# Optimization experiments

Hardware: AMD Instinct MI355X
Metric: run time of the kernel (lower is better)

## Reference

```python
import jax, jax.numpy as jnp
import numpy as np

L_IMG, L_TXT, B, C, T, D = 12, 12, 64, 1000, 8, 512


def setup_inputs() -> dict:
    key = jax.random.key(0)
    ks = jax.random.split(key, 8)
    s = 0.05  # keep attention logits in a sane range
    return {
        "x": jax.random.normal(ks[0], (L_IMG, B, D), jnp.float32),                 # per-layer projected CLS feats [L,B,D]
        "text_features": jax.random.normal(ks[1], (C, L_TXT, T, D), jnp.float32),  # precomputed per-class text feats
        "self_in_w": jax.random.normal(ks[2], (3 * D, D), jnp.float32) * s,
        "self_in_b": jnp.zeros((3 * D,), jnp.float32),
        "self_out_w": jax.random.normal(ks[3], (D, D), jnp.float32) * s,
        "self_out_b": jnp.zeros((D,), jnp.float32),
        "cross_in_w": jax.random.normal(ks[4], (3 * D, D), jnp.float32) * s,
        "cross_in_b": jnp.zeros((3 * D,), jnp.float32),
        "cross_out_w": jax.random.normal(ks[5], (D, D), jnp.float32) * s,
        "cross_out_b": jnp.zeros((D,), jnp.float32),
        "logit_scale": jnp.full((1,), np.log(1.0 / 0.07), jnp.float32),
    }


def reference(x, text_features, self_in_w, self_in_b, self_out_w, self_out_b,
              cross_in_w, cross_in_b, cross_out_w, cross_out_b, logit_scale):
    d = x.shape[-1]
    scale = 1.0 / jnp.sqrt(jnp.asarray(d, x.dtype))

    # ---- self-attention over the layer axis (torch MHA, 1 head, seq-first [L,B,D]) ----
    Wq, Wk, Wv = jnp.split(self_in_w, 3, axis=0)
    bq, bk, bv = jnp.split(self_in_b, 3, axis=0)
    q = jnp.einsum('lbd,ed->lbe', x, Wq) + bq
    k = jnp.einsum('lbd,ed->lbe', x, Wk) + bk
    v = jnp.einsum('lbd,ed->lbe', x, Wv) + bv
    attn = jax.nn.softmax(jnp.einsum('lbe,mbe->blm', q, k) * scale, axis=-1)
    xs = jnp.einsum('blm,mbe->lbe', attn, v) @ self_out_w.T + self_out_b   # [L,B,D]
    image_features = xs[-1]                                               # [B,D]

    # ---- batched cross-attention: query = image layer-tokens, key/value = per-class,
    #      per-template text layer-tokens; averaged over templates and query layers ----
    cWq, cWk, cWv = jnp.split(cross_in_w, 3, axis=0)
    cbq, cbk, cbv = jnp.split(cross_in_b, 3, axis=0)
    q2 = jnp.einsum('lbd,ed->lbe', xs, cWq) + cbq                          # [L,B,E]
    k2 = jnp.einsum('cmtd,ed->cmte', text_features, cWk) + cbk             # [C,M,T,E]
    v2 = jnp.einsum('cmtd,ed->cmte', text_features, cWv) + cbv
    a2 = jax.nn.softmax(jnp.einsum('lbe,cmte->bctlm', q2, k2) * scale, axis=-1)
    n_avg = a2.shape[2] * a2.shape[3]                                      # T * L_img
    # out_proj is linear, so mean over (template, layer) commutes with it
    ctx = jnp.einsum('bctlm,cmtd->bcd', a2, v2) / n_avg                    # [B,C,D]
    txt = ctx @ cross_out_w.T + cross_out_b                                # [B,C,D]

    # ---- normalize and compute logits (matching the source's permute(1,2,0) + norm(dim=-1)) ----
    tf = jnp.transpose(txt, (0, 2, 1))                                     # [B,D,C]
    img_n = image_features / jnp.linalg.norm(image_features, axis=-1, keepdims=True)
    tf_n = tf / jnp.linalg.norm(tf, axis=-1, keepdims=True)
    return jnp.exp(logit_scale[0]) * jnp.einsum('bd,bdc->bc', img_n, tf_n)  # [B,C]
```

## Files before the change

### kernel.cpp

```cpp
#include <hip/hip_runtime.h>

#define L_IMG 12
#define BATCH 64
#define NCLS  1000
#define DIM   512
#define NTM   96
#define SCALEF 0.044194173824159216f

typedef __attribute__((ext_vector_type(8))) short bf16x8;
typedef __attribute__((ext_vector_type(4))) float f32x4;

__device__ __forceinline__ float bf2f(unsigned short u) {
    return __uint_as_float(((unsigned int)u) << 16);
}
__device__ __forceinline__ unsigned short f2bf(float f) {
    unsigned int u = __float_as_uint(f);
    u += 0x7FFFu + ((u >> 16) & 1u);
    return (unsigned short)(u >> 16);
}
__device__ __forceinline__ void storeo(float* p, float v) { *p = v; }
__device__ __forceinline__ void storeo(unsigned short* p, float v) { *p = f2bf(v); }

__device__ __forceinline__ int swz(int row, int u) {
    return (row << 5) + ((u ^ ((row >> 1) & 3)) << 3);
}

__device__ __forceinline__ void gload16(const unsigned short* g, unsigned short* l) {
    __builtin_amdgcn_global_load_lds(
        (const __attribute__((address_space(1))) void*)g,
        (__attribute__((address_space(3))) void*)l, 16, 0, 0);
}

__global__ __launch_bounds__(256)
void f2bf_kernel(const float* __restrict__ in, unsigned short* __restrict__ out, int n)
{
    int i = (blockIdx.x * 256 + threadIdx.x) * 4;
    if (i < n) {
        float4 v = *(const float4*)(in + i);
        ushort4 o;
        o.x = f2bf(v.x); o.y = f2bf(v.y); o.z = f2bf(v.z); o.w = f2bf(v.w);
        *(ushort4*)(out + i) = o;
    }
}

__global__ __launch_bounds__(256)
void fold_wvo(const float* __restrict__ cow, const float* __restrict__ cWv,
              const float* __restrict__ cbv, const float* __restrict__ cob,
              unsigned short* __restrict__ Wvob, float* __restrict__ bvo)
{
    __shared__ float crow[DIM];
    __shared__ float red[256];
    const int d = blockIdx.x, t = threadIdx.x;
    float c0 = cow[d * DIM + t], c1 = cow[d * DIM + t + 256];
    crow[t] = c0; crow[t + 256] = c1;
    red[t] = c0 * cbv[t] + c1 * cbv[t + 256];
    __syncthreads();
    for (int s = 128; s > 0; s >>= 1) {
        if (t < s) red[t] += red[t + s];
        __syncthreads();
    }
    if (t == 0) bvo[d] = red[0] + cob[d];
    float a0 = 0.f, a1 = 0.f;
    for (int e = 0; e < DIM; e++) {
        float ce = crow[e];
        a0 += ce * cWv[e * DIM + t];
        a1 += ce * cWv[e * DIM + t + 256];
    }
    Wvob[d * DIM + t]       = f2bf(a0);
    Wvob[d * DIM + t + 256] = f2bf(a1);
}

#define BKT 32
#define LDT 68
__global__ __launch_bounds__(256)
void gemm_bt_f32(const float* __restrict__ A, const float* __restrict__ W,
                 const float* __restrict__ bias, float* __restrict__ Co,
                 int M, int N, int K, float out_scale)
{
    __shared__ float As[BKT * LDT];
    __shared__ float Ws[BKT * LDT];
    const int tid = threadIdx.x;
    const int m0 = blockIdx.y << 6, n0 = blockIdx.x << 6;
    const int tx = tid & 15, ty = tid >> 4;
    float acc[4][4] = {};
    for (int k0 = 0; k0 < K; k0 += BKT) {
        #pragma unroll
        for (int i = 0; i < 2; i++) {
            int slot = tid + (i << 8);
            int r = slot >> 3, kq = slot & 7;
            float4 v = *(const float4*)(A + (size_t)(m0 + r) * K + k0 + (kq << 2));
            As[(kq*4+0)*LDT + r] = v.x; As[(kq*4+1)*LDT + r] = v.y;
            As[(kq*4+2)*LDT + r] = v.z; As[(kq*4+3)*LDT + r] = v.w;
            float4 w = *(const float4*)(W + (size_t)(n0 + r) * K + k0 + (kq << 2));
            Ws[(kq*4+0)*LDT + r] = w.x; Ws[(kq*4+1)*LDT + r] = w.y;
            Ws[(kq*4+2)*LDT + r] = w.z; Ws[(kq*4+3)*LDT + r] = w.w;
        }
        __syncthreads();
        #pragma unroll
        for (int kk = 0; kk < BKT; kk++) {
            float4 a = *(const float4*)(As + kk*LDT + ty*4);
            float4 w = *(const float4*)(Ws + kk*LDT + tx*4);
            acc[0][0] += a.x*w.x; acc[0][1] += a.x*w.y; acc[0][2] += a.x*w.z; acc[0][3] += a.x*w.w;
            acc[1][0] += a.y*w.x; acc[1][1] += a.y*w.y; acc[1][2] += a.y*w.z; acc[1][3] += a.y*w.w;
            acc[2][0] += a.z*w.x; acc[2][1] += a.z*w.y; acc[2][2] += a.z*w.z; acc[2][3] += a.z*w.w;
            acc[3][0] += a.w*w.x; acc[3][1] += a.w*w.y; acc[3][2] += a.w*w.z; acc[3][3] += a.w*w.w;
        }
        __syncthreads();
    }
    #pragma unroll
    for (int i = 0; i < 4; i++) {
        int mr = m0 + ty*4 + i;
        #pragma unroll
        for (int j = 0; j < 4; j++) {
            int n = n0 + tx*4 + j;
            float v = acc[i][j];
            if (bias) v += bias[n];
            Co[(size_t)mr * N + n] = v * out_scale;
        }
    }
}

__global__ __launch_bounds__(256)
void gemm_nt_f32(const float* __restrict__ A, const float* __restrict__ W,
                 float* __restrict__ Co, int M, int N, int K)
{
    __shared__ float As[BKT * LDT];
    __shared__ float Ws[BKT * LDT];
    const int tid = threadIdx.x;
    const int m0 = blockIdx.y << 6, n0 = blockIdx.x << 6;
    const int tx = tid & 15, ty = tid >> 4;
    float acc[4][4] = {};
    for (int k0 = 0; k0 < K; k0 += BKT) {
        #pragma unroll
        for (int i = 0; i < 2; i++) {
            int slot = tid + (i << 8);
            int r = slot >> 3, kq = slot & 7;
            float4 v = *(const float4*)(A + (size_t)(m0 + r) * K + k0 + (kq << 2));
            As[(kq*4+0)*LDT + r] = v.x; As[(kq*4+1)*LDT + r] = v.y;
            As[(kq*4+2)*LDT + r] = v.z; As[(kq*4+3)*LDT + r] = v.w;
            int kr = slot >> 4, c4 = slot & 15;
            *(float4*)(Ws + kr*LDT + c4*4) =
                *(const float4*)(W + (size_t)(k0 + kr) * N + n0 + (c4 << 2));
        }
        __syncthreads();
        #pragma unroll
        for (int kk = 0; kk < BKT; kk++) {
            float4 a = *(const float4*)(As + kk*LDT + ty*4);
            float4 w = *(const float4*)(Ws + kk*LDT + tx*4);
            acc[0][0] += a.x*w.x; acc[0][1] += a.x*w.y; acc[0][2] += a.x*w.z; acc[0][3] += a.x*w.w;
            acc[1][0] += a.y*w.x; acc[1][1] += a.y*w.y; acc[1][2] += a.y*w.z; acc[1][3] += a.y*w.w;
            acc[2][0] += a.z*w.x; acc[2][1] += a.z*w.y; acc[2][2] += a.z*w.z; acc[2][3] += a.z*w.w;
            acc[3][0] += a.w*w.x; acc[3][1] += a.w*w.y; acc[3][2] += a.w*w.z; acc[3][3] += a.w*w.w;
        }
        __syncthreads();
    }
    #pragma unroll
    for (int i = 0; i < 4; i++) {
        int mr = m0 + ty*4 + i;
        #pragma unroll
        for (int j = 0; j < 4; j++)
            Co[(size_t)mr * N + n0 + tx*4 + j] = acc[i][j];
    }
}

__global__ __launch_bounds__(256)
void attn_kernel(const float* __restrict__ qkv, float* __restrict__ ao)
{
    __shared__ float lq[L_IMG * DIM];
    __shared__ float lk[L_IMG * DIM];
    __shared__ float sc[L_IMG * L_IMG];
    __shared__ float sa[L_IMG * L_IMG];
    const int b = blockIdx.x, tid = threadIdx.x;
    for (int i = 0; i < 6; i++) {
        int slot = tid + (i << 8);
        int l = slot >> 7, e4 = slot & 127;
        const float* row = qkv + (size_t)(l * BATCH + b) * 1536;
        *(float4*)(lq + l*DIM + e4*4) = *(const float4*)(row + e4*4);
        *(float4*)(lk + l*DIM + e4*4) = *(const float4*)(row + DIM + e4*4);
    }
    __syncthreads();
    if (tid < 144) {
        int l = tid / 12, m = tid % 12;
        float a = 0.f;
        for (int d4 = 0; d4 < 128; d4++) {
            float4 q = *(const float4*)(lq + l*DIM + d4*4);
            float4 k = *(const float4*)(lk + m*DIM + d4*4);
            a += q.x*k.x + q.y*k.y + q.z*k.z + q.w*k.w;
        }
        sc[tid] = a * SCALEF;
    }
    __syncthreads();
    if (tid < 12) {
        float mx = -1e30f;
        for (int m = 0; m < 12; m++) mx = fmaxf(mx, sc[tid*12 + m]);
        float e[12], s = 0.f;
        for (int m = 0; m < 12; m++) { e[m] = __expf(sc[tid*12 + m] - mx); s += e[m]; }
        float inv = 1.f / s;
        for (int m = 0; m < 12; m++) sa[tid*12 + m] = e[m] * inv;
    }
    __syncthreads();
    for (int i = 0; i < 2; i++) {
        int e = tid + (i << 8);
        float vv[12];
        #pragma unroll
        for (int m = 0; m < 12; m++)
            vv[m] = qkv[(size_t)(m * BATCH + b) * 1536 + 1024 + e];
        #pragma unroll
        for (int l = 0; l < 12; l++) {
            float a = 0.f;
            #pragma unroll
            for (int m = 0; m < 12; m++) a += sa[l*12 + m] * vv[m];
            ao[(size_t)(l * BATCH + b) * DIM + e] = a;
        }
    }
}

__global__ __launch_bounds__(256)
void img_kernel(const float* __restrict__ xs, float* __restrict__ imgn)
{
    __shared__ float red[256];
    const int b = blockIdx.x, tid = threadIdx.x;
    const float* row = xs + (size_t)(11 * BATCH + b) * DIM;
    float v0 = row[tid], v1 = row[tid + 256];
    red[tid] = v0*v0 + v1*v1;
    __syncthreads();
    for (int s = 128; s > 0; s >>= 1) {
        if (tid < s) red[tid] += red[tid + s];
        __syncthreads();
    }
    float inv = rsqrtf(red[0]);
    imgn[b*DIM + tid]       = v0 * inv;
    imgn[b*DIM + tid + 256] = v1 * inv;
}

__global__ __launch_bounds__(256)
void build_q2p(const float* __restrict__ q2s, unsigned short* __restrict__ q2pb)
{
    const int l = blockIdx.x, b = blockIdx.y, t = threadIdx.x;
    int d0 = t * 2;
    unsigned int o = 0;
    if (l < 12) {
        float2 v = *(const float2*)(q2s + (size_t)(l * BATCH + b) * DIM + d0);
        o = (unsigned int)f2bf(v.x) | ((unsigned int)f2bf(v.y) << 16);
    }
    ((unsigned int*)q2pb)[(size_t)(b * 16 + l) * 256 + t] = o;
}

template<typename OutT>
__global__ __launch_bounds__(256, 4)
void gemm_mfma(const unsigned short* __restrict__ A, const unsigned short* __restrict__ W,
               const float* __restrict__ bias, OutT* __restrict__ Co,
               int M, int N, float scale)
{
    const int K = DIM;
    __shared__ __align__(16) unsigned short AsBuf[2][128 * 32];
    __shared__ __align__(16) unsigned short WsBuf[2][128 * 32];
    const int m0 = blockIdx.y << 7, n0 = blockIdx.x << 7;
    const int tid = threadIdx.x;
    const int w = tid >> 6, lane = tid & 63;
    const int mt0 = (w & 1) * 4, nt0 = (w >> 1) * 4;
    const int r16 = lane & 15, kq = lane >> 4;
    const int row0 = (w << 5) + (lane >> 2), row1 = row0 + 16;
    const int sc0 = ((lane & 3) ^ ((row0 >> 1) & 3)) << 3;
    const int sc1 = ((lane & 3) ^ ((row1 >> 1) & 3)) << 3;
    const unsigned short* gA0 = A + (size_t)(m0 + row0) * K + sc0;
    const unsigned short* gA1 = A + (size_t)(m0 + row1) * K + sc1;
    const unsigned short* gW0 = W + (size_t)(n0 + row0) * K + sc0;
    const unsigned short* gW1 = W + (size_t)(n0 + row1) * K + sc1;
    const int lw = w << 10;
    int offa[4], offb[4];
    #pragma unroll
    for (int i = 0; i < 4; i++) {
        offa[i] = swz((mt0 + i) * 16 + r16, kq);
        offb[i] = swz((nt0 + i) * 16 + r16, kq);
    }
    f32x4 acc[4][4] = {};

    gload16(gA0, AsBuf[0] + lw);
    gload16(gA1, AsBuf[0] + lw + 512);
    gload16(gW0, WsBuf[0] + lw);
    gload16(gW1, WsBuf[0] + lw + 512);
    __syncthreads();

    #pragma unroll
    for (int t = 0; t < 16; t++) {
        const int cur = t & 1, nxt = cur ^ 1;
        if (t < 15) {
            const int ko = (t + 1) << 5;
            gload16(gA0 + ko, AsBuf[nxt] + lw);
            gload16(gA1 + ko, AsBuf[nxt] + lw + 512);
            gload16(gW0 + ko, WsBuf[nxt] + lw);
            gload16(gW1 + ko, WsBuf[nxt] + lw + 512);
        }
        bf16x8 af[4], bfr[4];
        #pragma unroll
        for (int i = 0; i < 4; i++) {
            af[i]  = *(const bf16x8*)(AsBuf[cur] + offa[i]);
            bfr[i] = *(const bf16x8*)(WsBuf[cur] + offb[i]);
        }
        #pragma unroll
        for (int i = 0; i < 4; i++)
            #pragma unroll
            for (int j = 0; j < 4; j++)
                acc[i][j] = __builtin_amdgcn_mfma_f32_16x16x32_bf16(af[i], bfr[j], acc[i][j], 0, 0, 0);
        if (t < 15) __syncthreads();
    }
    const int rbase = (lane >> 4) * 4;
    #pragma unroll
    for (int i = 0; i < 4; i++)
        #pragma unroll
        for (int j = 0; j < 4; j++) {
            int gcol = n0 + (nt0 + j) * 16 + r16;
            float bv = bias ? bias[gcol] : 0.f;
            #pragma unroll
            for (int r = 0; r < 4; r++) {
                int grow = m0 + (mt0 + i) * 16 + rbase + r;
                storeo(Co + (size_t)grow * N + gcol, acc[i][j][r] * scale + bv);
            }
        }
}

__global__ __launch_bounds__(256, 5)
void fused_scores(const unsigned short* __restrict__ q2pb, const unsigned short* __restrict__ k2,
                  float* __restrict__ wout)
{
    __shared__ __align__(16) unsigned short AsBuf[2][128 * 32];
    __shared__ __align__(16) unsigned short KsBuf[2][96 * 32];
    const int bid = blockIdx.x;
    const int g = bid >> 6, r = bid & 63;
    const int c = g * 8 + (r & 7), bg = r >> 3;
    const int tid = threadIdx.x;
    const int m0 = bg << 7;
    const int w = tid >> 6, lane = tid & 63;
    const int mt0 = w * 2;
    const int r16 = lane & 15, kq = lane >> 4;
    const size_t kb = (size_t)c * NTM * DIM;
    const int row0 = (w << 5) + (lane >> 2), row1 = row0 + 16;
    const int sc0 = ((lane & 3) ^ ((row0 >> 1) & 3)) << 3;
    const int sc1 = ((lane & 3) ^ ((row1 >> 1) & 3)) << 3;
    const unsigned short* gA0 = q2pb + (size_t)(m0 + row0) * DIM + sc0;
    const unsigned short* gA1 = q2pb + (size_t)(m0 + row1) * DIM + sc1;
    const unsigned short* gK0 = k2 + kb + (size_t)row0 * DIM + sc0;
    const unsigned short* gK1 = k2 + kb + (size_t)row1 * DIM + sc1;
    const bool kw = (w < 3);
    const int lw = w << 10;
    int offa[2], offk[6];
    #pragma unroll
    for (int i = 0; i < 2; i++) offa[i] = swz((mt0 + i) * 16 + r16, kq);
    #pragma unroll
    for (int j = 0; j < 6; j++) offk[j] = swz(j * 16 + r16, kq);
    f32x4 acc[2][6] = {};

    gload16(gA0, AsBuf[0] + lw);
    gload16(gA1, AsBuf[0] + lw + 512);
    if (kw) {
        gload16(gK0, KsBuf[0] + lw);
        gload16(gK1, KsBuf[0] + lw + 512);
    }
    __syncthreads();

    #pragma unroll
    for (int t = 0; t < 16; t++) {
        const int cur = t & 1, nxt = cur ^ 1;
        if (t < 15) {
            const int ko = (t + 1) << 5;
            gload16(gA0 + ko, AsBuf[nxt] + lw);
            gload16(gA1 + ko, AsBuf[nxt] + lw + 512);
            if (kw) {
                gload16(gK0 + ko, KsBuf[nxt] + lw);
                gload16(gK1 + ko, KsBuf[nxt] + lw + 512);
            }
        }
        bf16x8 af[2], bfr[6];
        #pragma unroll
        for (int i = 0; i < 2; i++)
            af[i] = *(const bf16x8*)(AsBuf[cur] + offa[i]);
        #pragma unroll
        for (int j = 0; j < 6; j++)
            bfr[j] = *(const bf16x8*)(KsBuf[cur] + offk[j]);
        __builtin_amdgcn_s_setprio(1);
        #pragma unroll
        for (int j = 0; j < 6; j++) {
            acc[0][j] = __builtin_amdgcn_mfma_f32_16x16x32_bf16(af[0], bfr[j], acc[0][j], 0, 0, 0);
            acc[1][j] = __builtin_amdgcn_mfma_f32_16x16x32_bf16(af[1], bfr[j], acc[1][j], 0, 0, 0);
        }
        __builtin_amdgcn_s_setprio(0);
        if (t < 15) __syncthreads();
    }

    #pragma unroll
    for (int i = 0; i < 2; i++) {
        #pragma unroll
        for (int rr = 0; rr < 4; rr++) {
            float v0 = acc[i][0][rr], v1 = acc[i][1][rr], v2 = acc[i][2][rr];
            float v3 = acc[i][3][rr], v4 = acc[i][4][rr], v5 = acc[i][5][rr];
            float mx = fmaxf(fmaxf(fmaxf(v0, v1), fmaxf(v2, v3)), fmaxf(v4, v5));
            mx = fmaxf(mx, __shfl_xor(mx, 8, 64));
            float e0 = __expf(v0 - mx), e1 = __expf(v1 - mx), e2 = __expf(v2 - mx);
            float e3 = __expf(v3 - mx), e4 = __expf(v4 - mx), e5 = __expf(v5 - mx);
            float s = e0 + e1 + e2 + e3 + e4 + e5;
            s += __shfl_xor(s, 8, 64);
            float inv = 1.f / (96.f * s);
            acc[i][0][rr] = e0 * inv; acc[i][1][rr] = e1 * inv; acc[i][2][rr] = e2 * inv;
            acc[i][3][rr] = e3 * inv; acc[i][4][rr] = e4 * inv; acc[i][5][rr] = e5 * inv;
        }
    }

    const bool contrib = (lane >> 4) < 3;
    #pragma unroll
    for (int i = 0; i < 2; i++) {
        float s6[6];
        #pragma unroll
        for (int j = 0; j < 6; j++) {
            float t = contrib ? (acc[i][j][0] + acc[i][j][1] + acc[i][j][2] + acc[i][j][3]) : 0.f;
            t += __shfl_xor(t, 16, 64);
            t += __shfl_xor(t, 32, 64);
            s6[j] = t;
        }
        if (lane < 16) {
            const int b = bg * 8 + mt0 + i;
            float* dst = wout + ((size_t)(b * NCLS + c)) * NTM;
            #pragma unroll
            for (int j = 0; j < 6; j++)
                dst[j * 16 + r16] = s6[j];
        }
    }
}

__global__ __launch_bounds__(256)
void ctx_kernel(const float* __restrict__ wbuf, const unsigned short* __restrict__ tfeb,
                unsigned short* __restrict__ ctxraw)
{
    __shared__ float ws[16 * NTM];
    const int bid = blockIdx.x;
    const int g = bid >> 5, r = bid & 31;
    const int c = g * 8 + (r & 7), bg = r >> 3;
    const int tid = threadIdx.x;
    for (int idx = tid; idx < 16 * NTM; idx += 256) {
        int bl = idx / NTM, tm = idx - bl * NTM;
        ws[idx] = wbuf[((size_t)((bg * 16 + bl) * NCLS + c)) * NTM + tm];
    }
    __syncthreads();
    float a0[16] = {}, a1[16] = {};
    const unsigned int* vrow = (const unsigned int*)(tfeb + (size_t)c * NTM * DIM) + tid;
    for (int tm = 0; tm < NTM; tm++) {
        unsigned int u = vrow[tm * 256];
        float vx = __uint_as_float(u << 16);
        float vy = __uint_as_float(u & 0xFFFF0000u);
        #pragma unroll
        for (int bl = 0; bl < 16; bl++) {
            float wv = ws[bl * NTM + tm];
            a0[bl] += wv * vx; a1[bl] += wv * vy;
        }
    }
    #pragma unroll
    for (int bl = 0; bl < 16; bl++) {
        int b = bg * 16 + bl;
        unsigned int o = (unsigned int)f2bf(a0[bl]) | ((unsigned int)f2bf(a1[bl]) << 16);
        ((unsigned int*)ctxraw)[(size_t)(b * NCLS + c) * 256 + tid] = o;
    }
}

__global__ __launch_bounds__(256)
void n2_kernel(const unsigned short* __restrict__ txt, float* __restrict__ n2)
{
    const int b = blockIdx.x, cg = blockIdx.y, t = threadIdx.x;
    float a0 = 0.f, a1 = 0.f;
    const unsigned int* p = (const unsigned int*)txt + ((size_t)(b * NCLS + cg * 125)) * 256 + t;
    for (int c = 0; c < 125; c++) {
        unsigned int u = p[c * 256];
        float vx = __uint_as_float(u << 16);
        float vy = __uint_as_float(u & 0xFFFF0000u);
        a0 += vx * vx; a1 += vy * vy;
    }
    atomicAdd(&n2[b * DIM + t * 2], a0);
    atomicAdd(&n2[b * DIM + t * 2 + 1], a1);
}

__global__ __launch_bounds__(256)
void logits_kernel(const unsigned short* __restrict__ txt, const float* __restrict__ imgn,
                   const float* __restrict__ n2, const float* __restrict__ logit_scale,
                   float* __restrict__ out)
{
    __shared__ float lu[DIM];
    const int b = blockIdx.y, cg = blockIdx.x, tid = threadIdx.x;
    float els = expf(logit_scale[0]);
    lu[tid]       = els * imgn[b*DIM + tid]       * rsqrtf(n2[b*DIM + tid]);
    lu[tid + 256] = els * imgn[b*DIM + tid + 256] * rsqrtf(n2[b*DIM + tid + 256]);
    __syncthreads();
    int wave = tid >> 6, lane = tid & 63;
    int c = (cg << 2) + wave;
    const unsigned short* row = txt + (size_t)(b * NCLS + c) * DIM;
    ushort4 p0 = ((const ushort4*)row)[lane*2];
    ushort4 p1 = ((const ushort4*)row)[lane*2 + 1];
    int d0 = lane * 8;
    float s = bf2f(p0.x)*lu[d0]   + bf2f(p0.y)*lu[d0+1] + bf2f(p0.z)*lu[d0+2] + bf2f(p0.w)*lu[d0+3]
            + bf2f(p1.x)*lu[d0+4] + bf2f(p1.y)*lu[d0+5] + bf2f(p1.z)*lu[d0+6] + bf2f(p1.w)*lu[d0+7];
    #pragma unroll
    for (int off = 32; off > 0; off >>= 1) s += __shfl_down(s, off, 64);
    if (lane == 0) out[b*NCLS + c] = s;
}

extern "C" void kernel_launch(void* const* d_in, const int* in_sizes, int n_in,
                              void* d_out, int out_size, void* d_ws, size_t ws_size,
                              hipStream_t stream)
{
    const float* x   = (const float*)d_in[0];
    const float* tfe = (const float*)d_in[1];
    const float* siw = (const float*)d_in[2];
    const float* sib = (const float*)d_in[3];
    const float* sow = (const float*)d_in[4];
    const float* sob = (const float*)d_in[5];
    const float* ciw = (const float*)d_in[6];
    const float* cib = (const float*)d_in[7];
    const float* cow = (const float*)d_in[8];
    const float* cob = (const float*)d_in[9];
    const float* ls  = (const float*)d_in[10];
    float* out = (float*)d_out;

    char* p = (char*)d_ws;
    auto alloc = [&](size_t bytes) { char* r = p; p += (bytes + 255) & ~255ull; return r; };
    unsigned short* tfeb   = (unsigned short*)alloc((size_t)49152000 * 2);
    unsigned short* ctxraw = (unsigned short*)alloc((size_t)BATCH * NCLS * DIM * 2);
    float* wbuf            = (float*)alloc((size_t)BATCH * NCLS * NTM * 4);
    float* qkv             = (float*)alloc((size_t)768 * 1536 * 4);
    float* ao              = (float*)alloc((size_t)768 * DIM * 4);
    float* xs              = (float*)alloc((size_t)768 * DIM * 4);
    float* q2s             = (float*)alloc((size_t)768 * DIM * 4);
    float* q2k             = (float*)alloc((size_t)768 * DIM * 4);
    unsigned short* q2pb   = (unsigned short*)alloc((size_t)1024 * DIM * 2);
    unsigned short* Wvob   = (unsigned short*)alloc((size_t)DIM * DIM * 2);
    float* bvo             = (float*)alloc(DIM * 4);
    float* n2              = (float*)alloc(BATCH * DIM * 4);
    float* imgn            = (float*)alloc(BATCH * DIM * 4);
    unsigned short* txt    = tfeb;

    hipMemsetAsync(n2, 0, BATCH * DIM * 4, stream);

    f2bf_kernel<<<48000, 256, 0, stream>>>(tfe, tfeb, 49152000);
    fold_wvo<<<512, 256, 0, stream>>>(cow, ciw + 1024*512, cib + 1024, cob, Wvob, bvo);

    gemm_bt_f32<<<dim3(24, 12), 256, 0, stream>>>(x, siw, sib, qkv, 768, 1536, 512, 1.f);
    attn_kernel<<<64, 256, 0, stream>>>(qkv, ao);
    gemm_bt_f32<<<dim3(8, 12), 256, 0, stream>>>(ao, sow, sob, xs, 768, 512, 512, 1.f);
    img_kernel<<<64, 256, 0, stream>>>(xs, imgn);
    gemm_bt_f32<<<dim3(8, 12), 256, 0, stream>>>(xs, ciw, cib, q2s, 768, 512, 512, SCALEF);
    gemm_nt_f32<<<dim3(8, 12), 256, 0, stream>>>(q2s, ciw + 512*512, q2k, 768, 512, 512);
    build_q2p<<<dim3(16, 64), 256, 0, stream>>>(q2k, q2pb);

    fused_scores<<<8000, 256, 0, stream>>>(q2pb, tfeb, wbuf);

    ctx_kernel<<<4000, 256, 0, stream>>>(wbuf, tfeb, ctxraw);

    gemm_mfma<unsigned short><<<dim3(4, 500), 256, 0, stream>>>(
        ctxraw, Wvob, bvo, txt, 64000, 512, 1.f);

    n2_kernel<<<dim3(64, 8), 256, 0, stream>>>(txt, n2);
    logits_kernel<<<dim3(250, 64), 256, 0, stream>>>(txt, imgn, n2, ls, out);
}
```

Measured before the change: 793.1 us.

## Enlarge fused_scores batch tile to 256 rows and vectorize ctx weight reads

fused_scores now has each block handle 256 query rows (16 batches) per class instead of 128, with each wave computing 4x6 MFMA tiles. This halves the block count and the number of times each class's K tile is reloaded, which raises per-block register and LDS use and lowers occupancy (launch bounds go from 5 to 3 blocks per CU). ctx_kernel transposes its shared weight buffer to [tm][bl] so each step reads 16 weights with four float4 loads instead of 16 scalar reads, and unrolls the tm loop by 4.

New measurement: 762.7 us. 1.04x faster.

```diff
diff --git a/kernel.cpp b/kernel.cpp
--- a/kernel.cpp
+++ b/kernel.cpp
@@ -320,42 +320,48 @@
         }
 }
 
-__global__ __launch_bounds__(256, 5)
+__global__ __launch_bounds__(256, 3)
 void fused_scores(const unsigned short* __restrict__ q2pb, const unsigned short* __restrict__ k2,
                   float* __restrict__ wout)
 {
-    __shared__ __align__(16) unsigned short AsBuf[2][128 * 32];
+    __shared__ __align__(16) unsigned short AsBuf[2][256 * 32];
     __shared__ __align__(16) unsigned short KsBuf[2][96 * 32];
     const int bid = blockIdx.x;
-    const int g = bid >> 6, r = bid & 63;
+    const int g = bid >> 5, r = bid & 31;
     const int c = g * 8 + (r & 7), bg = r >> 3;
     const int tid = threadIdx.x;
-    const int m0 = bg << 7;
+    const int m0 = bg << 8;
     const int w = tid >> 6, lane = tid & 63;
-    const int mt0 = w * 2;
     const int r16 = lane & 15, kq = lane >> 4;
     const size_t kb = (size_t)c * NTM * DIM;
-    const int row0 = (w << 5) + (lane >> 2), row1 = row0 + 16;
-    const int sc0 = ((lane & 3) ^ ((row0 >> 1) & 3)) << 3;
-    const int sc1 = ((lane & 3) ^ ((row1 >> 1) & 3)) << 3;
-    const unsigned short* gA0 = q2pb + (size_t)(m0 + row0) * DIM + sc0;
-    const unsigned short* gA1 = q2pb + (size_t)(m0 + row1) * DIM + sc1;
-    const unsigned short* gK0 = k2 + kb + (size_t)row0 * DIM + sc0;
-    const unsigned short* gK1 = k2 + kb + (size_t)row1 * DIM + sc1;
+    const int arow = lane >> 2, aun = lane & 3;
+    const unsigned short* gAs[4];
+    #pragma unroll
+    for (int s = 0; s < 4; s++) {
+        int rw = (w << 6) + (s << 4) + arow;
+        int scx = (aun ^ ((rw >> 1) & 3)) << 3;
+        gAs[s] = q2pb + (size_t)(m0 + rw) * DIM + scx;
+    }
+    const int krow0 = (w << 5) + arow, krow1 = krow0 + 16;
+    const int sk0 = (aun ^ ((krow0 >> 1) & 3)) << 3;
+    const int sk1 = (aun ^ ((krow1 >> 1) & 3)) << 3;
+    const unsigned short* gK0 = k2 + kb + (size_t)krow0 * DIM + sk0;
+    const unsigned short* gK1 = k2 + kb + (size_t)krow1 * DIM + sk1;
     const bool kw = (w < 3);
-    const int lw = w << 10;
-    int offa[2], offk[6];
-    #pragma unroll
-    for (int i = 0; i < 2; i++) offa[i] = swz((mt0 + i) * 16 + r16, kq);
+    const int lwA = w << 11;
+    const int lwK = w << 10;
+    int offa[4], offk[6];
+    #pragma unroll
+    for (int i = 0; i < 4; i++) offa[i] = swz((w << 6) + i * 16 + r16, kq);
     #pragma unroll
     for (int j = 0; j < 6; j++) offk[j] = swz(j * 16 + r16, kq);
-    f32x4 acc[2][6] = {};
-
-    gload16(gA0, AsBuf[0] + lw);
-    gload16(gA1, AsBuf[0] + lw + 512);
+    f32x4 acc[4][6] = {};
+
+    #pragma unroll
+    for (int s = 0; s < 4; s++) gload16(gAs[s], AsBuf[0] + lwA + (s << 9));
     if (kw) {
-        gload16(gK0, KsBuf[0] + lw);
-        gload16(gK1, KsBuf[0] + lw + 512);
+        gload16(gK0, KsBuf[0] + lwK);
+        gload16(gK1, KsBuf[0] + lwK + 512);
     }
     __syncthreads();
 
@@ -364,32 +370,32 @@
         const int cur = t & 1, nxt = cur ^ 1;
         if (t < 15) {
             const int ko = (t + 1) << 5;
-            gload16(gA0 + ko, AsBuf[nxt] + lw);
-            gload16(gA1 + ko, AsBuf[nxt] + lw + 512);
+            #pragma unroll
+            for (int s = 0; s < 4; s++) gload16(gAs[s] + ko, AsBuf[nxt] + lwA + (s << 9));
             if (kw) {
-                gload16(gK0 + ko, KsBuf[nxt] + lw);
-                gload16(gK1 + ko, KsBuf[nxt] + lw + 512);
+                gload16(gK0 + ko, KsBuf[nxt] + lwK);
+                gload16(gK1 + ko, KsBuf[nxt] + lwK + 512);
             }
         }
-        bf16x8 af[2], bfr[6];
-        #pragma unroll
-        for (int i = 0; i < 2; i++)
+        bf16x8 af[4], bfr[6];
+        #pragma unroll
+        for (int i = 0; i < 4; i++)
             af[i] = *(const bf16x8*)(AsBuf[cur] + offa[i]);
         #pragma unroll
         for (int j = 0; j < 6; j++)
             bfr[j] = *(const bf16x8*)(KsBuf[cur] + offk[j]);
         __builtin_amdgcn_s_setprio(1);
         #pragma unroll
-        for (int j = 0; j < 6; j++) {
-            acc[0][j] = __builtin_amdgcn_mfma_f32_16x16x32_bf16(af[0], bfr[j], acc[0][j], 0, 0, 0);
-            acc[1][j] = __builtin_amdgcn_mfma_f32_16x16x32_bf16(af[1], bfr[j], acc[1][j], 0, 0, 0);
-        }
+        for (int i = 0; i < 4; i++)
+            #pragma unroll
+            for (int j = 0; j < 6; j++)
+                acc[i][j] = __builtin_amdgcn_mfma_f32_16x16x32_bf16(af[i], bfr[j], acc[i][j], 0, 0, 0);
         __builtin_amdgcn_s_setprio(0);
         if (t < 15) __syncthreads();
     }
 
     #pragma unroll
-    for (int i = 0; i < 2; i++) {
+    for (int i = 0; i < 4; i++) {
         #pragma unroll
         for (int rr = 0; rr < 4; rr++) {
             float v0 = acc[i][0][rr], v1 = acc[i][1][rr], v2 = acc[i][2][rr];
@@ -408,7 +414,7 @@
 
     const bool contrib = (lane >> 4) < 3;
     #pragma unroll
-    for (int i = 0; i < 2; i++) {
+    for (int i = 0; i < 4; i++) {
         float s6[6];
         #pragma unroll
         for (int j = 0; j < 6; j++) {
@@ -418,7 +424,7 @@
             s6[j] = t;
         }
         if (lane < 16) {
-            const int b = bg * 8 + mt0 + i;
+            const int b = bg * 16 + (w << 2) + i;
             float* dst = wout + ((size_t)(b * NCLS + c)) * NTM;
             #pragma unroll
             for (int j = 0; j < 6; j++)
@@ -431,26 +437,31 @@
 void ctx_kernel(const float* __restrict__ wbuf, const unsigned short* __restrict__ tfeb,
                 unsigned short* __restrict__ ctxraw)
 {
-    __shared__ float ws[16 * NTM];
+    __shared__ float ws[NTM * 16];
     const int bid = blockIdx.x;
     const int g = bid >> 5, r = bid & 31;
     const int c = g * 8 + (r & 7), bg = r >> 3;
     const int tid = threadIdx.x;
     for (int idx = tid; idx < 16 * NTM; idx += 256) {
         int bl = idx / NTM, tm = idx - bl * NTM;
-        ws[idx] = wbuf[((size_t)((bg * 16 + bl) * NCLS + c)) * NTM + tm];
+        ws[tm * 16 + bl] = wbuf[((size_t)((bg * 16 + bl) * NCLS + c)) * NTM + tm];
     }
     __syncthreads();
     float a0[16] = {}, a1[16] = {};
     const unsigned int* vrow = (const unsigned int*)(tfeb + (size_t)c * NTM * DIM) + tid;
+    #pragma unroll 4
     for (int tm = 0; tm < NTM; tm++) {
         unsigned int u = vrow[tm * 256];
         float vx = __uint_as_float(u << 16);
         float vy = __uint_as_float(u & 0xFFFF0000u);
+        float wq[16];
+        *(float4*)(wq + 0)  = *(const float4*)(ws + tm * 16 + 0);
+        *(float4*)(wq + 4)  = *(const float4*)(ws + tm * 16 + 4);
+        *(float4*)(wq + 8)  = *(const float4*)(ws + tm * 16 + 8);
+        *(float4*)(wq + 12) = *(const float4*)(ws + tm * 16 + 12);
         #pragma unroll
         for (int bl = 0; bl < 16; bl++) {
-            float wv = ws[bl * NTM + tm];
-            a0[bl] += wv * vx; a1[bl] += wv * vy;
+            a0[bl] += wq[bl] * vx; a1[bl] += wq[bl] * vy;
         }
     }
     #pragma unroll
@@ -548,7 +559,7 @@
     gemm_nt_f32<<<dim3(8, 12), 256, 0, stream>>>(q2s, ciw + 512*512, q2k, 768, 512, 512);
     build_q2p<<<dim3(16, 64), 256, 0, stream>>>(q2k, q2pb);
 
-    fused_scores<<<8000, 256, 0, stream>>>(q2pb, tfeb, wbuf);
+    fused_scores<<<4000, 256, 0, stream>>>(q2pb, tfeb, wbuf);
 
     ctx_kernel<<<4000, 256, 0, stream>>>(wbuf, tfeb, ctxraw);
 
```
